# Performance work log

Hardware: AMD Instinct MI355X
Metric: run time of the kernel (lower is better)

## Reference

```python
import jax, jax.numpy as jnp
import numpy as np

N_NODES = 100000
N_EDGES = 1600000
HIDDEN = 128
EDGE_DIM = 4
N_LAYERS = 3
IN_DIM = 2


def setup_inputs() -> dict:
    key = jax.random.key(0)
    ks = jax.random.split(key, 12)
    msg_in_dim = IN_DIM + HIDDEN + EDGE_DIM  # concat([V_pred, h]) gathered at senders + edge feats
    s = lambda fan_in: 1.0 / np.sqrt(fan_in)
    return {
        "P_Q_inj": jax.random.normal(ks[0], (N_NODES, IN_DIM), jnp.float32),
        "senders": jax.random.randint(ks[1], (N_EDGES,), 0, N_NODES, jnp.int32),
        "receivers": jax.random.randint(ks[2], (N_EDGES,), 0, N_NODES, jnp.int32),
        "edge_features": jax.random.normal(ks[3], (N_EDGES, EDGE_DIM), jnp.float32),
        "W_in": jax.random.normal(ks[4], (IN_DIM, HIDDEN), jnp.float32) * s(IN_DIM),
        "b_in": jnp.zeros((HIDDEN,), jnp.float32),
        "W_msg": jax.random.normal(ks[5], (N_LAYERS, msg_in_dim, HIDDEN), jnp.float32) * s(msg_in_dim),
        "b_msg": jnp.zeros((N_LAYERS, HIDDEN), jnp.float32),
        "W_out": jax.random.normal(ks[6], (N_LAYERS, HIDDEN, IN_DIM), jnp.float32) * s(HIDDEN),
        "b_out": jnp.zeros((N_LAYERS, IN_DIM), jnp.float32),
    }


def reference(P_Q_inj, senders, receivers, edge_features, W_in, b_in, W_msg, b_msg, W_out, b_out):
    N = P_Q_inj.shape[0]
    # initial voltage guess: magnitude 1, angle 0
    V_pred = jnp.zeros_like(P_Q_inj).at[:, 0].set(1.0)  # [N, 2]
    h = P_Q_inj @ W_in + b_in  # [N, H]
    for l in range(W_msg.shape[0]):
        node_inputs = jnp.concatenate([V_pred, h], axis=-1)  # [N, 2+H]
        # gather src feats, concat edge feats, dense message
        msg_in = jnp.concatenate([node_inputs[senders], edge_features], axis=-1)  # [E, 2+H+Fe]
        msg = msg_in @ W_msg[l] + b_msg[l]  # [E, H]
        # scatter-sum aggregate to receiver nodes
        agg = jax.ops.segment_sum(msg, receivers, num_segments=N)  # [N, H]
        h = jax.nn.relu(agg)
        delta_V = h @ W_out[l] + b_out[l]  # [N, 2]
        V_pred = V_pred + delta_V
    return V_pred
```

## Files before the change

### kernel.cpp

```cpp
#include <hip/hip_runtime.h>
#include <hip/hip_bf16.h>
#include <stdint.h>

#define H 128
#define NPB  224
#define NBK  448
#define BCAP 6144
#define NBLK 128

typedef __attribute__((ext_vector_type(8))) short bf16x8;
typedef __attribute__((ext_vector_type(4))) float f32x4;

__device__ __forceinline__ unsigned pack_bf16x2(float a, float b){
  unsigned ua = __float_as_uint(a);
  unsigned ub = __float_as_uint(b);
  unsigned ra = (ua + 0x7fffu + ((ua >> 16) & 1u)) >> 16;
  unsigned rb = (ub + 0x7fffu + ((ub >> 16) & 1u)) >> 16;
  return ra | (rb << 16);
}
__device__ __forceinline__ float bf_lo(unsigned u){ return __uint_as_float(u << 16); }
__device__ __forceinline__ float bf_hi(unsigned u){ return __uint_as_float(u & 0xffff0000u); }

__global__ void init_kernel(const float* __restrict__ PQ, const float* __restrict__ Win,
                            const float* __restrict__ bin, unsigned* __restrict__ h,
                            float* __restrict__ V, int N){
  int lane = threadIdx.x & 63;
  int wid  = (blockIdx.x * blockDim.x + threadIdx.x) >> 6;
  int nw   = (gridDim.x * blockDim.x) >> 6;
  int c0 = 2*lane, c1 = c0 + 1;
  float w00 = Win[c0], w01 = Win[c1], w10 = Win[H+c0], w11 = Win[H+c1];
  float b0 = bin[c0], b1 = bin[c1];
  for (int n = wid; n < N; n += nw){
    float p0 = PQ[2*n], p1 = PQ[2*n+1];
    float h0 = p0*w00 + p1*w10 + b0;
    float h1 = p0*w01 + p1*w11 + b1;
    h[(size_t)n*64 + lane] = pack_bf16x2(h0, h1);
    if (lane == 0){ V[2*n] = 1.0f; V[2*n+1] = 0.0f; }
  }
}

__global__ void countA_kernel(const int* __restrict__ recv, int* __restrict__ cmat, int E){
  __shared__ int hist[NBK];
  int t = threadIdx.x;
  for (int b = t; b < NBK; b += 256) hist[b] = 0;
  __syncthreads();
  int chunk = (E + NBLK - 1) / NBLK;
  int lo = blockIdx.x * chunk, hi = min(E, lo + chunk);
  for (int i = lo + t; i < hi; i += 256)
    atomicAdd(&hist[recv[i]/NPB], 1);
  __syncthreads();
  for (int b = t; b < NBK; b += 256) cmat[blockIdx.x*NBK + b] = hist[b];
}

__global__ void cscan_kernel(const int* __restrict__ cmat, int* __restrict__ gofs,
                             int* __restrict__ bbase, int* __restrict__ rowptr,
                             int NB, int N, int E){
  __shared__ int s[512];
  int t = threadIdx.x;
  int tot = 0;
  if (t < NB)
    for (int k = 0; k < NBLK; ++k) tot += cmat[k*NBK + t];
  s[t] = tot; __syncthreads();
  #pragma unroll
  for (int off = 1; off < 512; off <<= 1){
    int x = (t >= off) ? s[t-off] : 0;
    __syncthreads();
    s[t] += x;
    __syncthreads();
  }
  int run = s[t] - tot;
  if (t < NB){
    bbase[t] = run;
    for (int k = 0; k < NBLK; ++k){
      gofs[k*NBK + t] = run;
      run += cmat[k*NBK + t];
    }
  }
  if (t == 0){ bbase[NB] = E; rowptr[N] = E; }
}

__global__ void scatterC_kernel(const int* __restrict__ recv, const int* __restrict__ send,
                                const int* __restrict__ gofs,
                                unsigned long long* __restrict__ ebuf, int E){
  __shared__ int cur[NBK];
  int t = threadIdx.x;
  for (int b = t; b < NBK; b += 256) cur[b] = gofs[blockIdx.x*NBK + b];
  __syncthreads();
  int chunk = (E + NBLK - 1) / NBLK;
  int lo = blockIdx.x * chunk, hi = min(E, lo + chunk);
  for (int i = lo + t; i < hi; i += 256){
    int r = recv[i];
    int b = r / NPB;
    int rloc = r - b*NPB;
    int pos = atomicAdd(&cur[b], 1);
    ebuf[pos] = ((unsigned long long)(unsigned)send[i] << 32)
              | ((unsigned long long)(unsigned)rloc << 24)
              | (unsigned long long)(unsigned)i;
  }
}

__global__ void bsort_kernel(const unsigned long long* __restrict__ ebuf,
                             const int* __restrict__ bbase,
                             int* __restrict__ ssort, int* __restrict__ eid,
                             int* __restrict__ rowptr, int N, int NB){
  __shared__ unsigned long long se[BCAP];
  __shared__ int sdeg[256];
  __shared__ int scur[256];
  int b = blockIdx.x;
  int t = threadIdx.x;
  int base = bbase[b];
  int cnt  = bbase[b+1] - base;
  if (cnt > BCAP) cnt = BCAP;
  sdeg[t] = 0;
  __syncthreads();
  for (int i = t; i < cnt; i += 256){
    unsigned long long v = ebuf[base + i];
    se[i] = v;
    atomicAdd(&sdeg[(int)((v >> 24) & 0xFF)], 1);
  }
  __syncthreads();
  int own = sdeg[t];
  #pragma unroll
  for (int off = 1; off < 256; off <<= 1){
    int x = (t >= off) ? sdeg[t-off] : 0;
    __syncthreads();
    sdeg[t] += x;
    __syncthreads();
  }
  int excl = sdeg[t] - own;
  scur[t] = excl;
  int node0 = b*NPB;
  if (t < NPB && node0 + t < N) rowptr[node0 + t] = base + excl;
  __syncthreads();
  for (int i = t; i < cnt; i += 256){
    unsigned long long v = se[i];
    int off = atomicAdd(&scur[(int)((v >> 24) & 0xFF)], 1);
    ssort[base + off] = (int)(v >> 32);
    eid[base + off]   = (int)(v & 0xFFFFFF);
  }
}

__global__ void wprep_kernel(const float* __restrict__ Wmsg, unsigned* __restrict__ Wb, int L){
  int t = blockIdx.x*blockDim.x + threadIdx.x;
  if (t >= L*2048) return;
  int layer = t >> 11;
  int f = t & 2047;
  int ct   = f >> 8;
  int ks   = (f >> 6) & 3;
  int lane = f & 63;
  int col = ct*16 + (lane & 15);
  int kbase = ks*32 + (lane >> 4)*8;
  const float* Wl = Wmsg + (size_t)layer*134*H + 2*H;
  unsigned u0 = pack_bf16x2(Wl[(size_t)(kbase+0)*H + col], Wl[(size_t)(kbase+1)*H + col]);
  unsigned u1 = pack_bf16x2(Wl[(size_t)(kbase+2)*H + col], Wl[(size_t)(kbase+3)*H + col]);
  unsigned u2 = pack_bf16x2(Wl[(size_t)(kbase+4)*H + col], Wl[(size_t)(kbase+5)*H + col]);
  unsigned u3 = pack_bf16x2(Wl[(size_t)(kbase+6)*H + col], Wl[(size_t)(kbase+7)*H + col]);
  uint4* dst = reinterpret_cast<uint4*>(Wb) + (size_t)layer*2048 + f;
  *dst = make_uint4(u0, u1, u2, u3);
}

__global__ void node_msg_mfma(const float* __restrict__ V, const unsigned* __restrict__ h,
                              const float* __restrict__ Wmsg_l, const float* __restrict__ bmsg_l,
                              const unsigned* __restrict__ Wb_l, unsigned* __restrict__ msrc, int N){
  __shared__ uint4 wlds[2048];
  int tid = threadIdx.x;
  const uint4* wb4 = reinterpret_cast<const uint4*>(Wb_l);
  #pragma unroll
  for (int i = 0; i < 8; ++i) wlds[tid + 256*i] = wb4[tid + 256*i];
  __syncthreads();
  const bf16x8* wb = reinterpret_cast<const bf16x8*>(wlds);
  int lane = tid & 63;
  int gw   = (blockIdx.x*blockDim.x + tid) >> 6;
  int nwv  = (gridDim.x*blockDim.x) >> 6;
  int row = lane & 15, kg = lane >> 4;
  int ntiles = N >> 4;
  for (int t = gw; t < ntiles; t += nwv){
    int node0 = t << 4;
    const bf16x8* hrow = reinterpret_cast<const bf16x8*>(h + (size_t)(node0 + row)*64);
    bf16x8 a[4];
    #pragma unroll
    for (int ks = 0; ks < 4; ++ks) a[ks] = hrow[ks*4 + kg];
    float2 vv[4];
    #pragma unroll
    for (int r = 0; r < 4; ++r)
      vv[r] = *reinterpret_cast<const float2*>(V + 2*(node0 + kg*4 + r));
    #pragma unroll
    for (int ct = 0; ct < 8; ++ct){
      f32x4 acc = {0.f, 0.f, 0.f, 0.f};
      #pragma unroll
      for (int ks = 0; ks < 4; ++ks){
        bf16x8 b = wb[(ct*4 + ks)*64 + lane];
        acc = __builtin_amdgcn_mfma_f32_16x16x32_bf16(a[ks], b, acc, 0, 0, 0);
      }
      int col = ct*16 + row;
      float wv0 = Wmsg_l[col], wv1 = Wmsg_l[H + col], bb = bmsg_l[col];
      #pragma unroll
      for (int r = 0; r < 4; ++r){
        float o = acc[r] + vv[r].x*wv0 + vv[r].y*wv1 + bb;
        float oh = __shfl_xor(o, 1, 64);
        if (!(lane & 1)){
          int nr = node0 + kg*4 + r;
          msrc[(size_t)nr*64 + ct*8 + (row >> 1)] = pack_bf16x2(o, oh);
        }
      }
    }
  }
}

template<bool FIRST, bool WRITEH>
__global__ void agg_update_kernel(const unsigned* __restrict__ msrc,
                                  const int* __restrict__ rowptr,
                                  const int* __restrict__ eid,
                                  const int* __restrict__ ssort,
                                  const float* __restrict__ ef,
                                  const float* __restrict__ Wmsg_l,
                                  const float* __restrict__ Wout_l,
                                  const float* __restrict__ bout_l,
                                  const float* __restrict__ Vin,
                                  float* __restrict__ Vout,
                                  unsigned* __restrict__ h,
                                  float4* __restrict__ efsum, int N){
  int lane = threadIdx.x & 63;
  int wid  = (blockIdx.x*blockDim.x + threadIdx.x) >> 6;
  int nw   = (gridDim.x*blockDim.x) >> 6;
  int c0 = 2*lane, c1 = c0 + 1;
  float We00 = Wmsg_l[(size_t)130*H + c0], We01 = Wmsg_l[(size_t)130*H + c1];
  float We10 = Wmsg_l[(size_t)131*H + c0], We11 = Wmsg_l[(size_t)131*H + c1];
  float We20 = Wmsg_l[(size_t)132*H + c0], We21 = Wmsg_l[(size_t)132*H + c1];
  float We30 = Wmsg_l[(size_t)133*H + c0], We31 = Wmsg_l[(size_t)133*H + c1];
  float Wo00 = Wout_l[c0*2], Wo01 = Wout_l[c0*2+1];
  float Wo10 = Wout_l[c1*2], Wo11 = Wout_l[c1*2+1];
  float bo0 = bout_l[0], bo1 = bout_l[1];
  for (int n = wid; n < N; n += nw){
    int beg = rowptr[n], end = rowptr[n+1];
    float acc0 = 0.f, acc1 = 0.f;
    float sfx = 0.f, sfy = 0.f, sfz = 0.f, sfw = 0.f;
    for (int c = beg; c < end; c += 64){
      int inlane = (c + lane < end);
      int sv = inlane ? ssort[c + lane] : 0;
      if (FIRST && inlane){
        int e = eid[c + lane];
        float4 f = *reinterpret_cast<const float4*>(ef + (size_t)e*4);
        sfx += f.x; sfy += f.y; sfz += f.z; sfw += f.w;
      }
      int kmax = min(64, end - c);
      int j = 0;
      for (; j + 4 <= kmax; j += 4){
        int s0 = __shfl(sv, j,   64);
        int s1 = __shfl(sv, j+1, 64);
        int s2 = __shfl(sv, j+2, 64);
        int s3 = __shfl(sv, j+3, 64);
        unsigned u0 = msrc[(size_t)s0*64 + lane];
        unsigned u1 = msrc[(size_t)s1*64 + lane];
        unsigned u2 = msrc[(size_t)s2*64 + lane];
        unsigned u3 = msrc[(size_t)s3*64 + lane];
        acc0 += bf_lo(u0) + bf_lo(u1) + bf_lo(u2) + bf_lo(u3);
        acc1 += bf_hi(u0) + bf_hi(u1) + bf_hi(u2) + bf_hi(u3);
      }
      for (; j < kmax; ++j){
        int s = __shfl(sv, j, 64);
        unsigned u = msrc[(size_t)s*64 + lane];
        acc0 += bf_lo(u); acc1 += bf_hi(u);
      }
    }
    if (FIRST){
      #pragma unroll
      for (int off = 32; off > 0; off >>= 1){
        sfx += __shfl_xor(sfx, off, 64);
        sfy += __shfl_xor(sfy, off, 64);
        sfz += __shfl_xor(sfz, off, 64);
        sfw += __shfl_xor(sfw, off, 64);
      }
      if (lane == 0) efsum[n] = make_float4(sfx, sfy, sfz, sfw);
    } else {
      float4 f = efsum[n];
      sfx = f.x; sfy = f.y; sfz = f.z; sfw = f.w;
    }
    acc0 += sfx*We00 + sfy*We10 + sfz*We20 + sfw*We30;
    acc1 += sfx*We01 + sfy*We11 + sfz*We21 + sfw*We31;
    float a0 = fmaxf(acc0, 0.f), a1 = fmaxf(acc1, 0.f);
    if (WRITEH) h[(size_t)n*64 + lane] = pack_bf16x2(a0, a1);
    float p0 = a0*Wo00 + a1*Wo10;
    float p1 = a0*Wo01 + a1*Wo11;
    #pragma unroll
    for (int off = 32; off > 0; off >>= 1){
      p0 += __shfl_xor(p0, off, 64);
      p1 += __shfl_xor(p1, off, 64);
    }
    if (lane == 0){
      float v0 = Vin[2*n], v1 = Vin[2*n+1];
      Vout[2*n]   = v0 + p0 + bo0;
      Vout[2*n+1] = v1 + p1 + bo1;
    }
  }
}

extern "C" void kernel_launch(void* const* d_in, const int* in_sizes, int n_in,
                              void* d_out, int out_size, void* d_ws, size_t ws_size,
                              hipStream_t stream){
  const float* PQ      = (const float*)d_in[0];
  const int*   senders = (const int*)  d_in[1];
  const int*   recv    = (const int*)  d_in[2];
  const float* ef      = (const float*)d_in[3];
  const float* Win     = (const float*)d_in[4];
  const float* bin     = (const float*)d_in[5];
  const float* Wmsg    = (const float*)d_in[6];
  const float* bmsg    = (const float*)d_in[7];
  const float* Wout    = (const float*)d_in[8];
  const float* bout    = (const float*)d_in[9];
  int N = in_sizes[0] / 2;
  int E = in_sizes[1];
  int L = in_sizes[7] / H;
  int NB = (N + NPB - 1) / NPB;

  char* base = (char*)d_ws;
  size_t off = 0;
  auto alloc = [&](size_t bytes)->char*{
    char* p = base + off; off += (bytes + 255) & ~(size_t)255; return p;
  };
  unsigned* h      = (unsigned*)alloc((size_t)N*64*4);
  unsigned* msrc   = (unsigned*)alloc((size_t)N*64*4);
  float*    V      = (float*)   alloc((size_t)N*2*4);
  int*      rowptr = (int*)     alloc((size_t)(N+1)*4);
  int*      eid    = (int*)     alloc((size_t)E*4);
  int*      ssort  = (int*)     alloc((size_t)E*4);
  unsigned long long* ebuf = (unsigned long long*)alloc((size_t)E*8);
  float4*   efsum  = (float4*)  alloc((size_t)N*16);
  int*      cmat   = (int*)     alloc((size_t)NBLK*NBK*4);
  int*      gofs   = (int*)     alloc((size_t)NBLK*NBK*4);
  int*      bbase  = (int*)     alloc((size_t)(NB+1)*4);
  unsigned* Wb     = (unsigned*)alloc((size_t)L*2048*16);
  if (off > ws_size) return;

  init_kernel<<<2048, 256, 0, stream>>>(PQ, Win, bin, h, V, N);
  countA_kernel<<<NBLK, 256, 0, stream>>>(recv, cmat, E);
  cscan_kernel<<<1, 512, 0, stream>>>(cmat, gofs, bbase, rowptr, NB, N, E);
  scatterC_kernel<<<NBLK, 256, 0, stream>>>(recv, senders, gofs, ebuf, E);
  bsort_kernel<<<NB, 256, 0, stream>>>(ebuf, bbase, ssort, eid, rowptr, N, NB);
  wprep_kernel<<<(L*2048 + 255)/256, 256, 0, stream>>>(Wmsg, Wb, L);

  for (int l = 0; l < L; ++l){
    const float* Wmsg_l = Wmsg + (size_t)l*134*H;
    const float* bmsg_l = bmsg + (size_t)l*H;
    const float* Wout_l = Wout + (size_t)l*H*2;
    const float* bout_l = bout + (size_t)l*2;
    const unsigned* Wb_l = Wb + (size_t)l*2048*4;
    node_msg_mfma<<<784, 256, 0, stream>>>(V, h, Wmsg_l, bmsg_l, Wb_l, msrc, N);
    float* Vout = (l == L-1) ? (float*)d_out : V;
    if (l == 0)
      agg_update_kernel<true, true><<<2048, 256, 0, stream>>>(msrc, rowptr, eid, ssort, ef,
                                                        Wmsg_l, Wout_l, bout_l, V, Vout, h, efsum, N);
    else if (l < L-1)
      agg_update_kernel<false, true><<<2048, 256, 0, stream>>>(msrc, rowptr, eid, ssort, ef,
                                                         Wmsg_l, Wout_l, bout_l, V, Vout, h, efsum, N);
    else
      agg_update_kernel<false, false><<<2048, 256, 0, stream>>>(msrc, rowptr, eid, ssort, ef,
                                                         Wmsg_l, Wout_l, bout_l, V, Vout, h, efsum, N);
  }
}
```

Before: 445.6 us.

## Fold input projection into layer-0 message weights and skip first node GEMM

Layer 0's node features are an affine function of the two-dimensional P_Q input. The change precomputes a combined 2x128 matrix plus bias from W_in, b_in and the first message weights (including the constant V=(1,0) term), then writes the layer-0 per-node messages directly from P_Q. This removes the init kernel, the h buffer write/read and the first MFMA node-message GEMM. Layer 0 also now uses a constant initial V instead of reading it, and the rounding path changes from bf16 h times bf16 W to an fp32 fused product.

```diff
diff --git a/kernel.cpp b/kernel.cpp
--- a/kernel.cpp
+++ b/kernel.cpp
@@ -20,24 +20,6 @@
 }
 __device__ __forceinline__ float bf_lo(unsigned u){ return __uint_as_float(u << 16); }
 __device__ __forceinline__ float bf_hi(unsigned u){ return __uint_as_float(u & 0xffff0000u); }
-
-__global__ void init_kernel(const float* __restrict__ PQ, const float* __restrict__ Win,
-                            const float* __restrict__ bin, unsigned* __restrict__ h,
-                            float* __restrict__ V, int N){
-  int lane = threadIdx.x & 63;
-  int wid  = (blockIdx.x * blockDim.x + threadIdx.x) >> 6;
-  int nw   = (gridDim.x * blockDim.x) >> 6;
-  int c0 = 2*lane, c1 = c0 + 1;
-  float w00 = Win[c0], w01 = Win[c1], w10 = Win[H+c0], w11 = Win[H+c1];
-  float b0 = bin[c0], b1 = bin[c1];
-  for (int n = wid; n < N; n += nw){
-    float p0 = PQ[2*n], p1 = PQ[2*n+1];
-    float h0 = p0*w00 + p1*w10 + b0;
-    float h1 = p0*w01 + p1*w11 + b1;
-    h[(size_t)n*64 + lane] = pack_bf16x2(h0, h1);
-    if (lane == 0){ V[2*n] = 1.0f; V[2*n+1] = 0.0f; }
-  }
-}
 
 __global__ void countA_kernel(const int* __restrict__ recv, int* __restrict__ cmat, int E){
   __shared__ int hist[NBK];
@@ -157,6 +139,38 @@
   unsigned u3 = pack_bf16x2(Wl[(size_t)(kbase+6)*H + col], Wl[(size_t)(kbase+7)*H + col]);
   uint4* dst = reinterpret_cast<uint4*>(Wb) + (size_t)layer*2048 + f;
   *dst = make_uint4(u0, u1, u2, u3);
+}
+
+__global__ void prep0_kernel(const float* __restrict__ Wmsg, const float* __restrict__ bmsg,
+                             const float* __restrict__ Win, const float* __restrict__ bin,
+                             float* __restrict__ ACC){
+  int c = threadIdx.x;
+  const float* Wh = Wmsg + 2*H;
+  float a0 = 0.f, a1 = 0.f, cc = 0.f;
+  for (int k = 0; k < H; ++k){
+    float w = Wh[(size_t)k*H + c];
+    a0 += Win[k]     * w;
+    a1 += Win[H + k] * w;
+    cc += bin[k]     * w;
+  }
+  cc += Wmsg[c] + bmsg[c];
+  ACC[c] = a0; ACC[H + c] = a1; ACC[2*H + c] = cc;
+}
+
+__global__ void msrc0_kernel(const float* __restrict__ PQ, const float* __restrict__ ACC,
+                             unsigned* __restrict__ msrc, int N){
+  int lane = threadIdx.x & 63;
+  int wid  = (blockIdx.x*blockDim.x + threadIdx.x) >> 6;
+  int nw   = (gridDim.x*blockDim.x) >> 6;
+  int c0 = 2*lane, c1 = c0 + 1;
+  float A00 = ACC[c0], A01 = ACC[c1];
+  float A10 = ACC[H + c0], A11 = ACC[H + c1];
+  float C0  = ACC[2*H + c0], C1 = ACC[2*H + c1];
+  for (int n = wid; n < N; n += nw){
+    float2 pq = *reinterpret_cast<const float2*>(PQ + 2*n);
+    msrc[(size_t)n*64 + lane] = pack_bf16x2(pq.x*A00 + pq.y*A10 + C0,
+                                            pq.x*A01 + pq.y*A11 + C1);
+  }
 }
 
 __global__ void node_msg_mfma(const float* __restrict__ V, const unsigned* __restrict__ h,
@@ -283,12 +297,16 @@
     float p0 = a0*Wo00 + a1*Wo10;
     float p1 = a0*Wo01 + a1*Wo11;
     #pragma unroll
-    for (int off = 32; off > 0; off >>= 1){
+    for (int off = 16; off > 0; off >>= 1){
       p0 += __shfl_xor(p0, off, 64);
       p1 += __shfl_xor(p1, off, 64);
     }
+    p0 += __shfl_xor(p0, 32, 64);
+    p1 += __shfl_xor(p1, 32, 64);
     if (lane == 0){
-      float v0 = Vin[2*n], v1 = Vin[2*n+1];
+      float v0, v1;
+      if (FIRST){ v0 = 1.0f; v1 = 0.0f; }
+      else      { v0 = Vin[2*n]; v1 = Vin[2*n+1]; }
       Vout[2*n]   = v0 + p0 + bo0;
       Vout[2*n+1] = v1 + p1 + bo1;
     }
@@ -330,14 +348,16 @@
   int*      gofs   = (int*)     alloc((size_t)NBLK*NBK*4);
   int*      bbase  = (int*)     alloc((size_t)(NB+1)*4);
   unsigned* Wb     = (unsigned*)alloc((size_t)L*2048*16);
+  float*    ACC0   = (float*)   alloc((size_t)3*H*4);
   if (off > ws_size) return;
 
-  init_kernel<<<2048, 256, 0, stream>>>(PQ, Win, bin, h, V, N);
   countA_kernel<<<NBLK, 256, 0, stream>>>(recv, cmat, E);
   cscan_kernel<<<1, 512, 0, stream>>>(cmat, gofs, bbase, rowptr, NB, N, E);
   scatterC_kernel<<<NBLK, 256, 0, stream>>>(recv, senders, gofs, ebuf, E);
   bsort_kernel<<<NB, 256, 0, stream>>>(ebuf, bbase, ssort, eid, rowptr, N, NB);
   wprep_kernel<<<(L*2048 + 255)/256, 256, 0, stream>>>(Wmsg, Wb, L);
+  prep0_kernel<<<1, H, 0, stream>>>(Wmsg, bmsg, Win, bin, ACC0);
+  msrc0_kernel<<<2048, 256, 0, stream>>>(PQ, ACC0, msrc, N);
 
   for (int l = 0; l < L; ++l){
     const float* Wmsg_l = Wmsg + (size_t)l*134*H;
@@ -345,7 +365,8 @@
     const float* Wout_l = Wout + (size_t)l*H*2;
     const float* bout_l = bout + (size_t)l*2;
     const unsigned* Wb_l = Wb + (size_t)l*2048*4;
-    node_msg_mfma<<<784, 256, 0, stream>>>(V, h, Wmsg_l, bmsg_l, Wb_l, msrc, N);
+    if (l > 0)
+      node_msg_mfma<<<784, 256, 0, stream>>>(V, h, Wmsg_l, bmsg_l, Wb_l, msrc, N);
     float* Vout = (l == L-1) ? (float*)d_out : V;
     if (l == 0)
       agg_update_kernel<true, true><<<2048, 256, 0, stream>>>(msrc, rowptr, eid, ssort, ef,
```

Result: faster. 402.1 us (-9.7%).
